# Kernel optimization log

Measured on AMD Instinct MI355X. Metric: run time of the kernel, lower is better.

Reference implementation:

```python
import jax, jax.numpy as jnp
import numpy as np

# Static multi-level feature-map shapes (H, W) per level.
SPATIAL_SHAPES = np.array([[92, 160], [46, 80], [23, 40], [12, 20]], dtype=np.int32)
NUM_HEADS = 8
NUM_LEVELS = 4
NUM_POINTS = 4      # sampling points per head per level (num_all_points)
NUM_Z = 4           # num_Z_anchors; NUM_POINTS % NUM_Z == 0
EMBED = 256
HEAD_DIM = EMBED // NUM_HEADS


def setup_inputs() -> dict:
    key = jax.random.key(0)
    ks = jax.random.split(key, 10)
    bs, nq = 2, 10000
    nv = int((SPATIAL_SHAPES[:, 0] * SPATIAL_SHAPES[:, 1]).sum())  # 19560
    query = jax.random.normal(ks[0], (bs, nq, EMBED), jnp.float32)
    value = jax.random.normal(ks[1], (bs, nv, EMBED), jnp.float32)
    query_pos = jax.random.normal(ks[2], (bs, nq, EMBED), jnp.float32)
    reference_points = jax.random.uniform(ks[3], (bs, nq, NUM_Z, 2), jnp.float32)
    W_val = jax.random.normal(ks[4], (EMBED, EMBED), jnp.float32) / jnp.sqrt(EMBED)
    b_val = jnp.zeros((EMBED,), jnp.float32)
    W_off = jax.random.normal(ks[5], (EMBED, NUM_HEADS * NUM_LEVELS * NUM_POINTS * 2), jnp.float32) * 0.01
    b_off = jax.random.normal(ks[6], (NUM_HEADS * NUM_LEVELS * NUM_POINTS * 2,), jnp.float32) * 0.5
    W_attn = jax.random.normal(ks[7], (EMBED, NUM_HEADS * NUM_LEVELS * NUM_POINTS), jnp.float32) * 0.02
    b_attn = jnp.zeros((NUM_HEADS * NUM_LEVELS * NUM_POINTS,), jnp.float32)
    spatial_shapes = jnp.asarray(SPATIAL_SHAPES)
    return {
        'query': query, 'value': value, 'query_pos': query_pos,
        'reference_points': reference_points,
        'W_val': W_val, 'b_val': b_val, 'W_off': W_off, 'b_off': b_off,
        'W_attn': W_attn, 'b_attn': b_attn, 'spatial_shapes': spatial_shapes,
    }


def _bilinear(v, x, y, H, W):
    """grid_sample(mode='bilinear', padding_mode='zeros', align_corners=False).

    v: (bs, H, W, heads, d); x, y: (bs, nq, heads, P) pixel coords.
    Returns (bs, nq, heads, P, d).
    """
    x0 = jnp.floor(x)
    y0 = jnp.floor(y)
    wx1 = x - x0
    wy1 = y - y0
    wx0 = 1.0 - wx1
    wy0 = 1.0 - wy1
    x0i = x0.astype(jnp.int32)
    y0i = y0.astype(jnp.int32)
    b = jnp.arange(v.shape[0])[:, None, None, None]
    h = jnp.arange(v.shape[3])[None, None, :, None]

    def gather(yi, xi):
        valid = (yi >= 0) & (yi < H) & (xi >= 0) & (xi < W)
        yc = jnp.clip(yi, 0, H - 1)
        xc = jnp.clip(xi, 0, W - 1)
        g = v[b, yc, xc, h]  # (bs, nq, heads, P, d)
        return g * valid[..., None].astype(v.dtype)

    return (gather(y0i, x0i) * (wy0 * wx0)[..., None]
            + gather(y0i, x0i + 1) * (wy0 * wx1)[..., None]
            + gather(y0i + 1, x0i) * (wy1 * wx0)[..., None]
            + gather(y0i + 1, x0i + 1) * (wy1 * wx1)[..., None])


def reference(query, value, query_pos, reference_points, W_val, b_val,
              W_off, b_off, W_attn, b_attn, spatial_shapes):
    bs, nq, _ = query.shape
    q = query + query_pos
    # value projection -> per-head values
    v = (value @ W_val + b_val).reshape(bs, -1, NUM_HEADS, HEAD_DIM)
    # sampling offsets and attention weights from query
    off = (q @ W_off + b_off).reshape(bs, nq, NUM_HEADS, NUM_LEVELS, NUM_POINTS, 2)
    attn = (q @ W_attn + b_attn).reshape(bs, nq, NUM_HEADS, NUM_LEVELS * NUM_POINTS)
    attn = jax.nn.softmax(attn, axis=-1).reshape(bs, nq, NUM_HEADS, NUM_LEVELS, NUM_POINTS)
    # normalize offsets by (w, h) of each level
    norm = jnp.stack([spatial_shapes[:, 1], spatial_shapes[:, 0]], -1).astype(q.dtype)  # (L, 2)
    off = off / norm[None, None, None, :, None, :]
    # fold Z-anchor reference points in, matching the shape[-1]==2 branch
    off = off.reshape(bs, nq, NUM_HEADS, NUM_LEVELS, NUM_POINTS // NUM_Z, NUM_Z, 2)
    loc = reference_points[:, :, None, None, None, :, :] + off
    loc = loc.reshape(bs, nq, NUM_HEADS, NUM_LEVELS, NUM_POINTS, 2)
    grid = 2.0 * loc - 1.0  # grid_sample convention

    start = 0
    sampled = []
    for lvl in range(NUM_LEVELS):
        H, W = int(SPATIAL_SHAPES[lvl, 0]), int(SPATIAL_SHAPES[lvl, 1])
        vl = v[:, start:start + H * W].reshape(bs, H, W, NUM_HEADS, HEAD_DIM)
        start += H * W
        # align_corners=False pixel coords
        x = ((grid[:, :, :, lvl, :, 0] + 1.0) * W - 1.0) * 0.5
        y = ((grid[:, :, :, lvl, :, 1] + 1.0) * H - 1.0) * 0.5
        sampled.append(_bilinear(vl, x, y, H, W))
    samp = jnp.stack(sampled, axis=3)  # (bs, nq, heads, L, P, d)
    out = (samp * attn[..., None]).sum(axis=(3, 4))  # (bs, nq, heads, d)
    return out.reshape(bs, nq, NUM_HEADS * HEAD_DIM)
```

## Files before the change

### kernel.cpp

```cpp
#include <hip/hip_runtime.h>

#define NQ 10000
#define BS 2
#define NV 19560
#define NH 8
#define HD 32
#define EMB 256

typedef __attribute__((ext_vector_type(8))) short bf16x8;
typedef __attribute__((ext_vector_type(4))) float f32x4;

__device__ __forceinline__ unsigned short f2bf(float x) {
    unsigned u = __float_as_uint(x);
    u += 0x7FFFu + ((u >> 16) & 1u);
    return (unsigned short)(u >> 16);
}
__device__ __forceinline__ float bf2f(unsigned short h) {
    return __uint_as_float(((unsigned)h) << 16);
}

__global__ __launch_bounds__(256) void convert_val(const float* __restrict__ src,
                                                   ushort* __restrict__ dst) {
    size_t i = ((size_t)blockIdx.x * 256 + threadIdx.x) * 8;
    f32x4 a = *(const f32x4*)(src + i);
    f32x4 b = *(const f32x4*)(src + i + 4);
    ushort o[8];
    o[0]=f2bf(a.x); o[1]=f2bf(a.y); o[2]=f2bf(a.z); o[3]=f2bf(a.w);
    o[4]=f2bf(b.x); o[5]=f2bf(b.y); o[6]=f2bf(b.z); o[7]=f2bf(b.w);
    *(bf16x8*)(dst + i) = *(bf16x8*)o;
}

__global__ __launch_bounds__(256) void convert_q(const float* __restrict__ q,
                                                 const float* __restrict__ qp,
                                                 ushort* __restrict__ dst) {
    size_t i = ((size_t)blockIdx.x * 256 + threadIdx.x) * 8;
    f32x4 a = *(const f32x4*)(q + i)     + *(const f32x4*)(qp + i);
    f32x4 b = *(const f32x4*)(q + i + 4) + *(const f32x4*)(qp + i + 4);
    ushort o[8];
    o[0]=f2bf(a.x); o[1]=f2bf(a.y); o[2]=f2bf(a.z); o[3]=f2bf(a.w);
    o[4]=f2bf(b.x); o[5]=f2bf(b.y); o[6]=f2bf(b.z); o[7]=f2bf(b.w);
    *(bf16x8*)(dst + i) = *(bf16x8*)o;
}

__global__ __launch_bounds__(256) void convert_W(
    const float* __restrict__ Wv, const float* __restrict__ Wo,
    const float* __restrict__ Wa, const float* __restrict__ bv,
    const float* __restrict__ bo, const float* __restrict__ ba,
    ushort* __restrict__ Bh, ushort* __restrict__ Bl, float* __restrict__ bias) {
    int n = blockIdx.x;
    int k = threadIdx.x;
    float x;
    if (n < 256)       x = Wv[k * 256 + n];
    else if (n < 512)  x = Wo[k * 256 + (n - 256)];
    else               x = Wa[k * 128 + (n - 512)];
    unsigned short h = f2bf(x);
    Bh[n * 256 + k] = h;
    Bl[n * 256 + k] = f2bf(x - bf2f(h));
    if (k == 0)
        bias[n] = (n < 256) ? bv[n] : (n < 512) ? bo[n - 256] : ba[n - 512];
}

template<bool SPLITC>
__global__ __launch_bounds__(256) void mfma_gemm2(
    const ushort* __restrict__ A, const ushort* __restrict__ Bh_g,
    const ushort* __restrict__ Bl_g, const float* __restrict__ bias,
    ushort* __restrict__ Cv, float* __restrict__ C0, float* __restrict__ C1,
    int M)
{
    __shared__ short As[128][40], Bhs[128][40], Bls[128][40];

    const int tid = threadIdx.x;
    const int m0 = blockIdx.x * 128;
    const int n0 = blockIdx.y * 128;
    const int lane = tid & 63, wave = tid >> 6;
    const int wrow = (wave >> 1) * 64, wcol = (wave & 1) * 64;
    const int lr = lane & 15, quad = lane >> 4, lk = quad * 8;

    const int arow = tid >> 1;
    const int acol = (tid & 1) * 16;
    const bool aval = (m0 + arow) < M;
    const ushort* Ap  = A    + (size_t)(m0 + arow) * 256 + acol;
    const ushort* Bhp = Bh_g + (size_t)(n0 + arow) * 256 + acol;
    const ushort* Blp = Bl_g + (size_t)(n0 + arow) * 256 + acol;

    f32x4 acc[4][4] = {};

    for (int k0 = 0; k0 < 256; k0 += 32) {
        bf16x8 a0 = {}, a1 = {};
        if (aval) {
            a0 = *(const bf16x8*)(Ap + k0);
            a1 = *(const bf16x8*)(Ap + k0 + 8);
        }
        bf16x8 h0 = *(const bf16x8*)(Bhp + k0);
        bf16x8 h1 = *(const bf16x8*)(Bhp + k0 + 8);
        bf16x8 l0 = *(const bf16x8*)(Blp + k0);
        bf16x8 l1 = *(const bf16x8*)(Blp + k0 + 8);
        *(bf16x8*)&As[arow][acol]      = a0;
        *(bf16x8*)&As[arow][acol + 8]  = a1;
        *(bf16x8*)&Bhs[arow][acol]     = h0;
        *(bf16x8*)&Bhs[arow][acol + 8] = h1;
        *(bf16x8*)&Bls[arow][acol]     = l0;
        *(bf16x8*)&Bls[arow][acol + 8] = l1;
        __syncthreads();

        bf16x8 af[4], bhf[4], blf[4];
        #pragma unroll
        for (int i = 0; i < 4; i++)
            af[i] = *(const bf16x8*)&As[wrow + i * 16 + lr][lk];
        #pragma unroll
        for (int j = 0; j < 4; j++) {
            bhf[j] = *(const bf16x8*)&Bhs[wcol + j * 16 + lr][lk];
            blf[j] = *(const bf16x8*)&Bls[wcol + j * 16 + lr][lk];
        }
        #pragma unroll
        for (int i = 0; i < 4; i++)
            #pragma unroll
            for (int j = 0; j < 4; j++) {
                acc[i][j] = __builtin_amdgcn_mfma_f32_16x16x32_bf16(af[i], bhf[j], acc[i][j], 0, 0, 0);
                acc[i][j] = __builtin_amdgcn_mfma_f32_16x16x32_bf16(af[i], blf[j], acc[i][j], 0, 0, 0);
            }
        __syncthreads();
    }

    #pragma unroll
    for (int j = 0; j < 4; j++) {
        int cc = wcol + j * 16 + lr;
        int col = n0 + cc;
        float bb = bias[col];
        #pragma unroll
        for (int i = 0; i < 4; i++) {
            int gmb = m0 + wrow + i * 16 + quad * 4;
            #pragma unroll
            for (int r = 0; r < 4; r++) {
                int gm = gmb + r;
                if (gm < M) {
                    float val = acc[i][j][r] + bb;
                    if (!SPLITC) {
                        int h = col >> 5, d = col & 31;
                        int b = (gm >= NV) ? 1 : 0;
                        int pix = gm - b * NV;
                        Cv[((size_t)(b * 8 + h) * NV + pix) * 32 + d] = f2bf(val);
                    } else {
                        if (col < 256) C0[(size_t)gm * 256 + col] = val;
                        else           C1[(size_t)gm * 128 + (col - 256)] = val;
                    }
                }
            }
        }
    }
}

__global__ __launch_bounds__(256) void sample2(
    const ushort* __restrict__ v, const float* __restrict__ off,
    const float* __restrict__ attn, const float* __restrict__ refp,
    float* __restrict__ out)
{
    __shared__ int   s_off[128][5];
    __shared__ float s_w[128][5];

    const int bq = blockIdx.x;
    const int b = (bq >= NQ) ? 1 : 0;
    const int t = threadIdx.x;

    if (t < 128) {
        const int h = t >> 4, i = t & 15, l = i >> 2, p = i & 3;
        float logit = attn[(size_t)bq * 128 + t];
        float mx = logit;
        #pragma unroll
        for (int m = 1; m < 16; m <<= 1) mx = fmaxf(mx, __shfl_xor(mx, m, 16));
        float e = __expf(logit - mx);
        float s = e;
        #pragma unroll
        for (int m = 1; m < 16; m <<= 1) s += __shfl_xor(s, m, 16);
        float w = e / s;

        const float Wf[4] = {160.f, 80.f, 40.f, 20.f};
        const float Hf[4] = {92.f, 46.f, 23.f, 12.f};
        const int   Wi[4] = {160, 80, 40, 20};
        const int   Hi[4] = {92, 46, 23, 12};
        const int   st[4] = {0, 14720, 18400, 19320};

        float ox = off[(size_t)bq * 256 + h * 32 + l * 8 + p * 2];
        float oy = off[(size_t)bq * 256 + h * 32 + l * 8 + p * 2 + 1];
        float rx = refp[(size_t)bq * 8 + p * 2];
        float ry = refp[(size_t)bq * 8 + p * 2 + 1];
        float x = rx * Wf[l] + ox - 0.5f;
        float y = ry * Hf[l] + oy - 0.5f;
        float x0f = floorf(x), y0f = floorf(y);
        float wx1 = x - x0f, wy1 = y - y0f;
        float wx0 = 1.f - wx1, wy0 = 1.f - wy1;
        int x0 = (int)x0f, y0 = (int)y0f;
        const int W = Wi[l], H = Hi[l];
        float mx0 = ((unsigned)x0       < (unsigned)W) ? 1.f : 0.f;
        float mx1 = ((unsigned)(x0 + 1) < (unsigned)W) ? 1.f : 0.f;
        float my0 = ((unsigned)y0       < (unsigned)H) ? 1.f : 0.f;
        float my1 = ((unsigned)(y0 + 1) < (unsigned)H) ? 1.f : 0.f;
        int xc0 = min(max(x0, 0), W - 1);
        int xc1 = min(max(x0 + 1, 0), W - 1);
        int yc0 = min(max(y0, 0), H - 1);
        int yc1 = min(max(y0 + 1, 0), H - 1);
        int base = ((b * 8 + h) * NV + st[l]) * 32;
        s_off[t][0] = base + (yc0 * W + xc0) * 32;
        s_off[t][1] = base + (yc0 * W + xc1) * 32;
        s_off[t][2] = base + (yc1 * W + xc0) * 32;
        s_off[t][3] = base + (yc1 * W + xc1) * 32;
        s_w[t][0] = w * wy0 * wx0 * my0 * mx0;
        s_w[t][1] = w * wy0 * wx1 * my0 * mx1;
        s_w[t][2] = w * wy1 * wx0 * my1 * mx0;
        s_w[t][3] = w * wy1 * wx1 * my1 * mx1;
    }
    __syncthreads();

    const int h = t >> 5, d = t & 31;
    float acc = 0.f;
    #pragma unroll 4
    for (int i = 0; i < 16; i++) {
        int idx = h * 16 + i;
        int o0 = s_off[idx][0], o1 = s_off[idx][1];
        int o2 = s_off[idx][2], o3 = s_off[idx][3];
        float w0 = s_w[idx][0], w1 = s_w[idx][1];
        float w2 = s_w[idx][2], w3 = s_w[idx][3];
        acc += w0 * bf2f(v[o0 + d]) + w1 * bf2f(v[o1 + d])
             + w2 * bf2f(v[o2 + d]) + w3 * bf2f(v[o3 + d]);
    }
    out[(size_t)bq * 256 + t] = acc;
}

extern "C" void kernel_launch(void* const* d_in, const int* in_sizes, int n_in,
                              void* d_out, int out_size, void* d_ws, size_t ws_size,
                              hipStream_t stream) {
    const float* query     = (const float*)d_in[0];
    const float* value     = (const float*)d_in[1];
    const float* query_pos = (const float*)d_in[2];
    const float* refp      = (const float*)d_in[3];
    const float* W_val     = (const float*)d_in[4];
    const float* b_val     = (const float*)d_in[5];
    const float* W_off     = (const float*)d_in[6];
    const float* b_off     = (const float*)d_in[7];
    const float* W_attn    = (const float*)d_in[8];
    const float* b_attn    = (const float*)d_in[9];
    float* out = (float*)d_out;

    char* w = (char*)d_ws;
    float*  off     = (float*)w;
    ushort* val_bf  = (ushort*)w;            w += 20480000;
    float*  attn    = (float*)w;             w += 10240000;
    ushort* qsum_bf = (ushort*)w;            w += 10240000;
    ushort* vp_bf   = (ushort*)w;            w += 20029440;
    ushort* Bt_hi   = (ushort*)w;            w += 327680;
    ushort* Bt_lo   = (ushort*)w;            w += 327680;
    float*  bias_c  = (float*)w;             w += 2560;

    const int Mv = BS * NV;
    const int Mq = BS * NQ;

    convert_val<<<4890, 256, 0, stream>>>(value, val_bf);
    convert_q<<<2500, 256, 0, stream>>>(query, query_pos, qsum_bf);
    convert_W<<<640, 256, 0, stream>>>(W_val, W_off, W_attn, b_val, b_off, b_attn,
                                       Bt_hi, Bt_lo, bias_c);

    dim3 gv((Mv + 127) / 128, 2);
    mfma_gemm2<false><<<gv, 256, 0, stream>>>(val_bf, Bt_hi, Bt_lo, bias_c,
                                              vp_bf, nullptr, nullptr, Mv);
    dim3 gq((Mq + 127) / 128, 3);
    mfma_gemm2<true><<<gq, 256, 0, stream>>>(qsum_bf, Bt_hi + 256 * 256,
                                             Bt_lo + 256 * 256, bias_c + 256,
                                             nullptr, off, attn, Mq);
    sample2<<<BS * NQ, 256, 0, stream>>>(vp_bf, off, attn, refp, out);
}
```

Before: 245.7 us.

## Drop bf16 split-weight correction and process two queries per sampling block

The weights are now converted to a single bf16 value, which removes the low-part residual, half the MFMA work and the extra B tile in shared memory in both projection GEMMs. The sampling kernel now handles two queries per 256-thread block, so all threads compute sampling offsets. Each thread gathers two adjacent bf16 channels with one 32-bit load and writes a float2. Dropping the residual term lowers weight precision, which may cost accuracy, especially for the offset projection that sets sampling locations.

```diff
diff --git a/kernel.cpp b/kernel.cpp
--- a/kernel.cpp
+++ b/kernel.cpp
@@ -46,16 +46,14 @@
     const float* __restrict__ Wv, const float* __restrict__ Wo,
     const float* __restrict__ Wa, const float* __restrict__ bv,
     const float* __restrict__ bo, const float* __restrict__ ba,
-    ushort* __restrict__ Bh, ushort* __restrict__ Bl, float* __restrict__ bias) {
+    ushort* __restrict__ Bh, float* __restrict__ bias) {
     int n = blockIdx.x;
     int k = threadIdx.x;
     float x;
     if (n < 256)       x = Wv[k * 256 + n];
     else if (n < 512)  x = Wo[k * 256 + (n - 256)];
     else               x = Wa[k * 128 + (n - 512)];
-    unsigned short h = f2bf(x);
-    Bh[n * 256 + k] = h;
-    Bl[n * 256 + k] = f2bf(x - bf2f(h));
+    Bh[n * 256 + k] = f2bf(x);
     if (k == 0)
         bias[n] = (n < 256) ? bv[n] : (n < 512) ? bo[n - 256] : ba[n - 512];
 }
@@ -63,11 +61,11 @@
 template<bool SPLITC>
 __global__ __launch_bounds__(256) void mfma_gemm2(
     const ushort* __restrict__ A, const ushort* __restrict__ Bh_g,
-    const ushort* __restrict__ Bl_g, const float* __restrict__ bias,
+    const float* __restrict__ bias,
     ushort* __restrict__ Cv, float* __restrict__ C0, float* __restrict__ C1,
     int M)
 {
-    __shared__ short As[128][40], Bhs[128][40], Bls[128][40];
+    __shared__ short As[128][40], Bhs[128][40];
 
     const int tid = threadIdx.x;
     const int m0 = blockIdx.x * 128;
@@ -81,7 +79,6 @@
     const bool aval = (m0 + arow) < M;
     const ushort* Ap  = A    + (size_t)(m0 + arow) * 256 + acol;
     const ushort* Bhp = Bh_g + (size_t)(n0 + arow) * 256 + acol;
-    const ushort* Blp = Bl_g + (size_t)(n0 + arow) * 256 + acol;
 
     f32x4 acc[4][4] = {};
 
@@ -93,32 +90,24 @@
         }
         bf16x8 h0 = *(const bf16x8*)(Bhp + k0);
         bf16x8 h1 = *(const bf16x8*)(Bhp + k0 + 8);
-        bf16x8 l0 = *(const bf16x8*)(Blp + k0);
-        bf16x8 l1 = *(const bf16x8*)(Blp + k0 + 8);
         *(bf16x8*)&As[arow][acol]      = a0;
         *(bf16x8*)&As[arow][acol + 8]  = a1;
         *(bf16x8*)&Bhs[arow][acol]     = h0;
         *(bf16x8*)&Bhs[arow][acol + 8] = h1;
-        *(bf16x8*)&Bls[arow][acol]     = l0;
-        *(bf16x8*)&Bls[arow][acol + 8] = l1;
         __syncthreads();
 
-        bf16x8 af[4], bhf[4], blf[4];
+        bf16x8 af[4], bhf[4];
         #pragma unroll
         for (int i = 0; i < 4; i++)
             af[i] = *(const bf16x8*)&As[wrow + i * 16 + lr][lk];
         #pragma unroll
-        for (int j = 0; j < 4; j++) {
+        for (int j = 0; j < 4; j++)
             bhf[j] = *(const bf16x8*)&Bhs[wcol + j * 16 + lr][lk];
-            blf[j] = *(const bf16x8*)&Bls[wcol + j * 16 + lr][lk];
-        }
         #pragma unroll
         for (int i = 0; i < 4; i++)
             #pragma unroll
-            for (int j = 0; j < 4; j++) {
+            for (int j = 0; j < 4; j++)
                 acc[i][j] = __builtin_amdgcn_mfma_f32_16x16x32_bf16(af[i], bhf[j], acc[i][j], 0, 0, 0);
-                acc[i][j] = __builtin_amdgcn_mfma_f32_16x16x32_bf16(af[i], blf[j], acc[i][j], 0, 0, 0);
-            }
         __syncthreads();
     }
 
@@ -150,21 +139,24 @@
     }
 }
 
-__global__ __launch_bounds__(256) void sample2(
+__global__ __launch_bounds__(256) void sample3(
     const ushort* __restrict__ v, const float* __restrict__ off,
     const float* __restrict__ attn, const float* __restrict__ refp,
     float* __restrict__ out)
 {
-    __shared__ int   s_off[128][5];
-    __shared__ float s_w[128][5];
-
-    const int bq = blockIdx.x;
-    const int b = (bq >= NQ) ? 1 : 0;
+    __shared__ int   s_off[256][5];
+    __shared__ float s_w[256][5];
+
+    const int bq0 = blockIdx.x * 2;
     const int t = threadIdx.x;
 
-    if (t < 128) {
-        const int h = t >> 4, i = t & 15, l = i >> 2, p = i & 3;
-        float logit = attn[(size_t)bq * 128 + t];
+    {
+        const int bq = bq0 + (t >> 7);
+        const int b = (bq >= NQ) ? 1 : 0;
+        const int i = t & 127;
+        const int h = i >> 4, l = (i >> 2) & 3, p = i & 3;
+
+        float logit = attn[(size_t)bq * 128 + i];
         float mx = logit;
         #pragma unroll
         for (int m = 1; m < 16; m <<= 1) mx = fmaxf(mx, __shfl_xor(mx, m, 16));
@@ -211,19 +203,28 @@
     }
     __syncthreads();
 
-    const int h = t >> 5, d = t & 31;
-    float acc = 0.f;
-    #pragma unroll 4
+    const int g = t >> 4;
+    const int lane = t & 15;
+    const int qi = g >> 3, h = g & 7;
+    const int bq = bq0 + qi;
+    const int d2 = lane * 2;
+
+    float accx = 0.f, accy = 0.f;
+    const int pbase = qi * 128 + h * 16;
+    #pragma unroll 8
     for (int i = 0; i < 16; i++) {
-        int idx = h * 16 + i;
-        int o0 = s_off[idx][0], o1 = s_off[idx][1];
-        int o2 = s_off[idx][2], o3 = s_off[idx][3];
-        float w0 = s_w[idx][0], w1 = s_w[idx][1];
-        float w2 = s_w[idx][2], w3 = s_w[idx][3];
-        acc += w0 * bf2f(v[o0 + d]) + w1 * bf2f(v[o1 + d])
-             + w2 * bf2f(v[o2 + d]) + w3 * bf2f(v[o3 + d]);
-    }
-    out[(size_t)bq * 256 + t] = acc;
+        int idx = pbase + i;
+        #pragma unroll
+        for (int c = 0; c < 4; c++) {
+            int o = s_off[idx][c];
+            float wgt = s_w[idx][c];
+            unsigned u = *(const unsigned*)(v + o + d2);
+            accx += wgt * __uint_as_float(u << 16);
+            accy += wgt * __uint_as_float(u & 0xffff0000u);
+        }
+    }
+    float2 res = make_float2(accx, accy);
+    *(float2*)(out + (size_t)bq * 256 + h * 32 + d2) = res;
 }
 
 extern "C" void kernel_launch(void* const* d_in, const int* in_sizes, int n_in,
@@ -248,7 +249,6 @@
     ushort* qsum_bf = (ushort*)w;            w += 10240000;
     ushort* vp_bf   = (ushort*)w;            w += 20029440;
     ushort* Bt_hi   = (ushort*)w;            w += 327680;
-    ushort* Bt_lo   = (ushort*)w;            w += 327680;
     float*  bias_c  = (float*)w;             w += 2560;
 
     const int Mv = BS * NV;
@@ -257,14 +257,14 @@
     convert_val<<<4890, 256, 0, stream>>>(value, val_bf);
     convert_q<<<2500, 256, 0, stream>>>(query, query_pos, qsum_bf);
     convert_W<<<640, 256, 0, stream>>>(W_val, W_off, W_attn, b_val, b_off, b_attn,
-                                       Bt_hi, Bt_lo, bias_c);
+                                       Bt_hi, bias_c);
 
     dim3 gv((Mv + 127) / 128, 2);
-    mfma_gemm2<false><<<gv, 256, 0, stream>>>(val_bf, Bt_hi, Bt_lo, bias_c,
+    mfma_gemm2<false><<<gv, 256, 0, stream>>>(val_bf, Bt_hi, bias_c,
                                               vp_bf, nullptr, nullptr, Mv);
     dim3 gq((Mq + 127) / 128, 3);
     mfma_gemm2<true><<<gq, 256, 0, stream>>>(qsum_bf, Bt_hi + 256 * 256,
-                                             Bt_lo + 256 * 256, bias_c + 256,
+                                             bias_c + 256,
                                              nullptr, off, attn, Mq);
-    sample2<<<BS * NQ, 256, 0, stream>>>(vp_bf, off, attn, refp, out);
-}
+    sample3<<<BS * NQ / 2, 256, 0, stream>>>(vp_bf, off, attn, refp, out);
+}
```

After: 258.2 us. 5.1% more time.
